# Optimization experiments

Measured on AMD Instinct MI355X. Metric: run time of the kernel, lower is better.

Reference implementation:

```python
import jax, jax.numpy as jnp
import numpy as np

DEPTH = 4
H1 = 64
H2 = 16
NF = 5
L = 10.0
K = 4
DIM = 3
N = 2048
NK = N // 4
FEAT = 1 + 2 * NF * DIM  # r scalar + Nf (cos,sin) pairs of dim components


def _tn(k, shape, std=0.01):
    return jax.random.truncated_normal(k, -2.0, 2.0, shape, jnp.float32) * std


def setup_inputs() -> dict:
    key = jax.random.key(0)
    ks = jax.random.split(key, 16)
    comb0 = 3 * DIM + 3 * FEAT   # combine width at depth 0
    combd = 3 * H1 + 3 * H2      # combine width at later depths
    return {
        "sx": jax.random.uniform(ks[0], (N, DIM), jnp.float32) * L,
        "kpoints": jax.random.normal(ks[1], (2 * NK, DIM), jnp.float32),
        "we0": _tn(ks[2], (comb0, H1)), "be0": jnp.zeros((H1,), jnp.float32),
        "we_rest": _tn(ks[3], (DEPTH - 1, combd, H1)), "be_rest": jnp.zeros((DEPTH - 1, H1), jnp.float32),
        "wee0": _tn(ks[4], (FEAT, H2)), "bee0": jnp.zeros((H2,), jnp.float32),
        "wee_rest": _tn(ks[5], (DEPTH - 2, H2, H2)), "bee_rest": jnp.zeros((DEPTH - 2, H2), jnp.float32),
        "wep0": _tn(ks[6], (FEAT, H2)), "bep0": jnp.zeros((H2,), jnp.float32),
        "wep_rest": _tn(ks[7], (DEPTH - 2, H2, H2)), "bep_rest": jnp.zeros((DEPTH - 2, H2), jnp.float32),
        "orb_w_re": _tn(ks[8], (H1, H1)), "orb_w_im": _tn(ks[9], (H1, H1)),
        "orb_b_re": jnp.zeros((H1,), jnp.float32), "orb_b_im": jnp.zeros((H1,), jnp.float32),
        "w_det": _tn(ks[10], (K, H1, H1)),
        "bf_w": _tn(ks[11], (H1, DIM)),
        "mlp_w1": _tn(ks[12], (DIM, H1)), "mlp_b1": jnp.zeros((H1,), jnp.float32),
        "mlp_w2": _tn(ks[13], (H1, K * (NK - 1))), "mlp_b2": jnp.zeros((K * (NK - 1),), jnp.float32),
    }


def _fourier(rij, r):
    # interleaved [r, cos1, sin1, ..., cosNf, sinNf] like the original
    feats = [r[..., None]]
    for k in range(1, NF + 1):
        ang = (2.0 * np.pi * k / L) * rij
        feats.append(jnp.cos(ang))
        feats.append(jnp.sin(ang))
    return jnp.concatenate(feats, axis=-1)


def _combine(e, ee, ep):
    mm = e.shape[0]
    h = mm // 2
    g1a = jnp.broadcast_to(jnp.mean(e[:h], 0, keepdims=True), e.shape)
    g1b = jnp.broadcast_to(jnp.mean(e[h:], 0, keepdims=True), e.shape)
    g2a = jnp.mean(ee[:h], axis=0)
    g2b = jnp.mean(ee[h:], axis=0)
    g3 = jnp.mean(ep, axis=1)
    return jnp.concatenate([e, g1a, g1b, g2a, g2b, g3], axis=1)


def _forward(sx, kpoints, we0, be0, we_rest, be_rest, wee0, bee0, wee_rest, bee_rest,
             wep0, bep0, wep_rest, bep_rest, orb_w_re, orb_w_im, orb_b_re, orb_b_im,
             w_det, bf_w, mlp_w1, mlp_b1, mlp_w2, mlp_b2):
    n, dim = sx.shape
    m, m2 = n // 2, n // 4
    s, x = sx[:m], sx[m:]
    e = jnp.broadcast_to(kpoints[0][None, :], (m, dim))
    # electron-electron pairwise features (m,m,FEAT)
    rij = x[:, None, :] - x[None, :, :]
    eye = jnp.eye(m, dtype=x.dtype)
    r = jnp.linalg.norm(jnp.sin(np.pi * rij / L) + eye[..., None], axis=-1) * (1.0 - eye) * (L / np.pi)
    ee = _fourier(rij, r)
    # electron-proton pairwise features (m,m,FEAT)
    rij = x[:, None, :] - s[None, :, :]
    r = jnp.linalg.norm(jnp.sin(np.pi * rij / L), axis=-1) * (L / np.pi)
    ep = _fourier(rij, r)
    for d in range(DEPTH - 1):
        f = _combine(e, ee, ep)
        We, be = (we0, be0) if d == 0 else (we_rest[d - 1], be_rest[d - 1])
        Wee, bee = (wee0, bee0) if d == 0 else (wee_rest[d - 1], bee_rest[d - 1])
        Wep, bep = (wep0, bep0) if d == 0 else (wep_rest[d - 1], bep_rest[d - 1])
        e_u = jnp.tanh(f @ We + be)
        ee_u = jnp.tanh(ee @ Wee + bee)
        ep_u = jnp.tanh(ep @ Wep + bep)
        e, ee, ep = (e_u + e, ee_u + ee, ep_u + ep) if d > 0 else (e_u, ee_u, ep_u)
    f = _combine(e, ee, ep)
    e = jnp.tanh(f @ we_rest[-1] + be_rest[-1]) + e
    # complex orbitals and geminal pairing matrix phi: (K, m2, m2)
    orb = e.astype(jnp.complex64) @ (orb_w_re + 1j * orb_w_im) + (orb_b_re + 1j * orb_b_im)
    phi = jnp.einsum('ia,kab,jb->kij', orb[:m2], w_det.astype(jnp.complex64), orb[m2:]) + 1.0
    # backflow coordinates and plane-wave determinant factors
    z = e @ bf_w + x
    nk = kpoints.shape[0] // 2
    norm = 1.0 / L ** (dim / 2)
    D_up = norm * jnp.exp(1j * jnp.einsum('kd,id->ki', kpoints[:nk], z[:m2]))  # (nk, m2)
    D_dn = norm * jnp.exp(1j * jnp.einsum('kd,id->ki', kpoints[nk:], z[m2:]))  # (nk, m2)
    h = jnp.tanh(kpoints[0] @ mlp_w1 + mlp_b1)
    fdet = jax.nn.softplus(h @ mlp_w2 + mlp_b2).reshape(K, nk - 1)
    fdet = jnp.concatenate([jnp.ones((K, 1), fdet.dtype), fdet], axis=1)  # (K, nk)
    D = jnp.einsum('ai,ka,aj->kij', D_up, fdet.astype(D_up.dtype), jnp.conj(D_dn))
    # logdet_matmul: stable log of signed sum of K determinants
    phase, logabs = jnp.linalg.slogdet(D * phi)
    maxl = jnp.max(logabs)
    det = jnp.sum(phase * jnp.exp(logabs - maxl))
    return jnp.log(jnp.abs(det)) + maxl + jnp.log(det / jnp.abs(det))


def reference(sx, kpoints, we0, be0, we_rest, be_rest, wee0, bee0, wee_rest, bee_rest,
              wep0, bep0, wep_rest, bep_rest, orb_w_re, orb_w_im, orb_b_re, orb_b_im,
              w_det, bf_w, mlp_w1, mlp_b1, mlp_w2, mlp_b2):
    return _forward(sx, kpoints, we0, be0, we_rest, be_rest, wee0, bee0, wee_rest, bee_rest,
                    wep0, bep0, wep_rest, bep_rest, orb_w_re, orb_w_im, orb_b_re, orb_b_im,
                    w_det, bf_w, mlp_w1, mlp_b1, mlp_w2, mlp_b2)
```

## Files before the change

kernel.cpp:

```cpp
#include <hip/hip_runtime.h>

typedef unsigned int uint;
typedef unsigned short ushort;

#define M1 1024
#define MH 512
#define PI_F 3.14159265358979323846f
#define LBOX 10.0f
#define NB 32

__device__ __forceinline__ float bf2f(ushort h){ return __uint_as_float(((uint)h)<<16); }
__device__ __forceinline__ ushort f2bf(float f){ uint u = __float_as_uint(f); uint r = (u + 0x7fffu + ((u>>16)&1u))>>16; return (ushort)r; }
__device__ __forceinline__ float ftanh(float x){ float e = __expf(2.f*x); return 1.f - 2.f/(e+1.f); }
__device__ __forceinline__ float2 cmul(float2 a, float2 b){ return make_float2(a.x*b.x - a.y*b.y, a.x*b.y + a.y*b.x); }
__device__ __forceinline__ void cfma(float2& c, float2 a, float2 b){
  c.x = fmaf(a.x,b.x,fmaf(-a.y,b.y,c.x));
  c.y = fmaf(a.x,b.y,fmaf(a.y,b.x,c.y));
}

__device__ __forceinline__ void fourier31(float d0, float d1, float d2, bool diag, float f[31]){
  const float k1 = PI_F / LBOX;
  float s[3], c[3];
  __sincosf(k1*d0, &s[0], &c[0]);
  __sincosf(k1*d1, &s[1], &c[1]);
  __sincosf(k1*d2, &s[2], &c[2]);
  float r = diag ? 0.f : (LBOX/PI_F)*sqrtf(s[0]*s[0]+s[1]*s[1]+s[2]*s[2]);
  f[0] = r;
  float cb[3], sb[3], cc[3], sc[3];
  #pragma unroll
  for (int d=0; d<3; ++d){ cb[d] = 1.f - 2.f*s[d]*s[d]; sb[d] = 2.f*s[d]*c[d]; cc[d]=cb[d]; sc[d]=sb[d]; }
  #pragma unroll
  for (int k=0;k<5;++k){
    #pragma unroll
    for (int d=0; d<3; ++d){ f[1+6*k+d] = cc[d]; f[4+6*k+d] = sc[d]; }
    if (k<4){
      #pragma unroll
      for (int d=0; d<3; ++d){
        float nc = cc[d]*cb[d]-sc[d]*sb[d];
        float ns = sc[d]*cb[d]+cc[d]*sb[d];
        cc[d]=nc; sc[d]=ns;
      }
    }
  }
}

__global__ void k_zero(float* __restrict__ p, int n){
  int i = blockIdx.x*256 + threadIdx.x;
  int st = gridDim.x*256;
  for (; i<n; i+=st) p[i] = 0.f;
}

__global__ void k_iota(int* __restrict__ rowmap){
  int q = blockIdx.x*256 + threadIdx.x;
  rowmap[q] = q & 511;
}

__global__ __launch_bounds__(256) void k_pair0(const float* __restrict__ sx, const float* __restrict__ W,
                                               const float* __restrict__ b, ushort* __restrict__ out, int is_ee,
                                               float* __restrict__ gA, float* __restrict__ gB){
  int bx = blockIdx.x;
  int i = bx >> 2;
  int chunk = bx & 3;
  int j = (chunk << 8) + threadIdx.x;
  const float* xs = sx + 3*M1;
  float xi0 = xs[3*i], xi1 = xs[3*i+1], xi2 = xs[3*i+2];
  const float* oth = is_ee ? xs : sx;
  float y0 = oth[3*j], y1 = oth[3*j+1], y2 = oth[3*j+2];
  float f[31];
  fourier31(xi0-y0, xi1-y1, xi2-y2, is_ee && (i==j), f);
  float acc[16];
  #pragma unroll
  for (int o=0;o<16;++o) acc[o] = b[o];
  #pragma unroll
  for (int c=0;c<31;++c){ float fv = f[c];
    #pragma unroll
    for (int o=0;o<16;++o) acc[o] = fmaf(fv, W[c*16+o], acc[o]);
  }
  uint u[8];
  #pragma unroll
  for (int h=0;h<8;++h){
    ushort lo = f2bf(ftanh(acc[2*h]));
    ushort hi = f2bf(ftanh(acc[2*h+1]));
    u[h] = (uint)lo | ((uint)hi<<16);
  }
  uint4* dst = (uint4*)(out + ((size_t)i*M1 + j)*16);
  dst[0] = make_uint4(u[0],u[1],u[2],u[3]);
  dst[1] = make_uint4(u[4],u[5],u[6],u[7]);
  __shared__ float buf[256*33];
  #pragma unroll
  for (int c=0;c<31;++c) buf[threadIdx.x*33+c] = f[c];
  __syncthreads();
  #pragma unroll
  for (int s=128; s>0; s>>=1){
    if (threadIdx.x < s){
      #pragma unroll
      for (int c=0;c<31;++c) buf[threadIdx.x*33+c] += buf[(threadIdx.x+s)*33+c];
    }
    __syncthreads();
  }
  if (threadIdx.x < 31){
    float* g = (is_ee && chunk >= 2) ? gB : gA;
    atomicAdd(&g[i*31+threadIdx.x], buf[threadIdx.x]);
  }
}

__global__ __launch_bounds__(256) void k_pairU(ushort* __restrict__ ten, const float* __restrict__ W,
                                               const float* __restrict__ b){
  size_t base = ((size_t)blockIdx.x*256 + threadIdx.x)*16;
  uint4 a0 = ((uint4*)(ten+base))[0];
  uint4 a1 = ((uint4*)(ten+base))[1];
  uint uu[8] = {a0.x,a0.y,a0.z,a0.w,a1.x,a1.y,a1.z,a1.w};
  float v[16];
  #pragma unroll
  for (int h=0;h<8;++h){ v[2*h] = bf2f((ushort)(uu[h]&0xffffu)); v[2*h+1] = bf2f((ushort)(uu[h]>>16)); }
  float acc[16];
  #pragma unroll
  for (int o=0;o<16;++o) acc[o] = b[o];
  #pragma unroll
  for (int c=0;c<16;++c){ float fv = v[c];
    #pragma unroll
    for (int o=0;o<16;++o) acc[o] = fmaf(fv, W[c*16+o], acc[o]);
  }
  uint w[8];
  #pragma unroll
  for (int h=0;h<8;++h){
    float q0 = ftanh(acc[2*h]) + v[2*h];
    float q1 = ftanh(acc[2*h+1]) + v[2*h+1];
    w[h] = (uint)f2bf(q0) | ((uint)f2bf(q1)<<16);
  }
  ((uint4*)(ten+base))[0] = make_uint4(w[0],w[1],w[2],w[3]);
  ((uint4*)(ten+base))[1] = make_uint4(w[4],w[5],w[6],w[7]);
}

__global__ __launch_bounds__(256) void k_gee(const ushort* __restrict__ ten, float* __restrict__ gA, float* __restrict__ gB){
  int jb = blockIdx.x >> 3;
  int ic = blockIdx.x & 7;
  int jl = threadIdx.x & 63;
  int iq = threadIdx.x >> 6;
  int j = jb*64 + jl;
  float acc[16];
  #pragma unroll
  for (int c=0;c<16;++c) acc[c]=0.f;
  for (int s=0;s<32;++s){
    int i = ic*128 + iq + 4*s;
    const uint4* src = (const uint4*)(ten + ((size_t)i*M1 + j)*16);
    uint4 a0 = src[0], a1 = src[1];
    uint uu[8]={a0.x,a0.y,a0.z,a0.w,a1.x,a1.y,a1.z,a1.w};
    #pragma unroll
    for (int h=0;h<8;++h){ acc[2*h]+=bf2f((ushort)(uu[h]&0xffffu)); acc[2*h+1]+=bf2f((ushort)(uu[h]>>16)); }
  }
  __shared__ float red[4][64][16];
  #pragma unroll
  for (int c=0;c<16;++c) red[iq][jl][c]=acc[c];
  __syncthreads();
  if (iq==0){
    float* out = (ic<4)? gA : gB;
    #pragma unroll
    for (int c=0;c<16;++c){
      float t = red[0][jl][c]+red[1][jl][c]+red[2][jl][c]+red[3][jl][c];
      atomicAdd(&out[j*16+c], t);
    }
  }
}

__global__ __launch_bounds__(256) void k_gep(const ushort* __restrict__ ten, float* __restrict__ g3){
  int ib = blockIdx.x;
  int il = threadIdx.x >> 6;
  int jl = threadIdx.x & 63;
  int i = ib*4 + il;
  float acc[16];
  #pragma unroll
  for (int c=0;c<16;++c) acc[c]=0.f;
  for (int s=0;s<16;++s){
    int j = jl + 64*s;
    const uint4* src = (const uint4*)(ten + ((size_t)i*M1 + j)*16);
    uint4 a0 = src[0], a1 = src[1];
    uint uu[8]={a0.x,a0.y,a0.z,a0.w,a1.x,a1.y,a1.z,a1.w};
    #pragma unroll
    for (int h=0;h<8;++h){ acc[2*h]+=bf2f((ushort)(uu[h]&0xffffu)); acc[2*h+1]+=bf2f((ushort)(uu[h]>>16)); }
  }
  __shared__ float red[4][64][16];
  #pragma unroll
  for (int c=0;c<16;++c) red[il][jl][c]=acc[c];
  __syncthreads();
  if (jl < 16){
    int c = jl;
    float t=0.f;
    for (int q=0;q<64;++q) t += red[il][q][c];
    g3[i*16+c] = t;
  }
}

__global__ __launch_bounds__(256) void k_e0(const float* __restrict__ kp, const float* __restrict__ g2a,
    const float* __restrict__ g2b, const float* __restrict__ g3, const float* __restrict__ W,
    const float* __restrict__ b, float* __restrict__ eout, float* __restrict__ g1out){
  int p = blockIdx.x*4 + (threadIdx.x>>6);
  int o = threadIdx.x & 63;
  float acc = b[o];
  #pragma unroll
  for (int d=0; d<3; ++d){
    acc = fmaf(kp[d], W[d*64+o] + W[(d+3)*64+o] + W[(d+6)*64+o], acc);
  }
  const float i512 = 1.f/512.f, i1024 = 1.f/1024.f;
  #pragma unroll
  for (int c=0;c<31;++c){
    float sg = (c!=0 && ((c-1)%6)>=3) ? -i512 : i512;
    acc = fmaf(g2a[p*31+c]*sg, W[(9+c)*64+o], acc);
  }
  #pragma unroll
  for (int c=0;c<31;++c){
    float sg = (c!=0 && ((c-1)%6)>=3) ? -i512 : i512;
    acc = fmaf(g2b[p*31+c]*sg, W[(40+c)*64+o], acc);
  }
  #pragma unroll
  for (int c=0;c<31;++c) acc = fmaf(g3[p*31+c]*i1024, W[(71+c)*64+o], acc);
  float v = ftanh(acc);
  eout[p*64+o] = v;
  atomicAdd(&g1out[(p<MH?0:64)+o], v);
}

__global__ __launch_bounds__(256) void k_eupd(const float* __restrict__ eprev, float* __restrict__ eout,
    const float* __restrict__ W, const float* __restrict__ b, const float* __restrict__ g1in,
    const float* __restrict__ g2a, const float* __restrict__ g2b, const float* __restrict__ g3,
    float* __restrict__ g1out){
  int p = blockIdx.x*4 + (threadIdx.x>>6);
  int o = threadIdx.x & 63;
  const float i512 = 1.f/512.f, i1024 = 1.f/1024.f;
  float acc = b[o];
  #pragma unroll 8
  for (int c=0;c<64;++c) acc = fmaf(eprev[p*64+c], W[c*64+o], acc);
  #pragma unroll 8
  for (int c=0;c<64;++c) acc = fmaf(g1in[c]*i512, W[(64+c)*64+o], acc);
  #pragma unroll 8
  for (int c=0;c<64;++c) acc = fmaf(g1in[64+c]*i512, W[(128+c)*64+o], acc);
  #pragma unroll
  for (int c=0;c<16;++c) acc = fmaf(g2a[p*16+c]*i512, W[(192+c)*64+o], acc);
  #pragma unroll
  for (int c=0;c<16;++c) acc = fmaf(g2b[p*16+c]*i512, W[(208+c)*64+o], acc);
  #pragma unroll
  for (int c=0;c<16;++c) acc = fmaf(g3[p*16+c]*i1024, W[(224+c)*64+o], acc);
  float v = ftanh(acc) + eprev[p*64+o];
  eout[p*64+o] = v;
  if (g1out) atomicAdd(&g1out[(p<MH?0:64)+o], v);
}

__global__ __launch_bounds__(256) void k_orbz(const float* __restrict__ e4, const float* __restrict__ Wre,
    const float* __restrict__ Wim, const float* __restrict__ bre, const float* __restrict__ bim,
    const float* __restrict__ bfw, const float* __restrict__ sx, float* __restrict__ ore,
    float* __restrict__ oim, float* __restrict__ z){
  int p = blockIdx.x*4 + (threadIdx.x>>6);
  int o = threadIdx.x & 63;
  float ar = bre[o], ai = bim[o];
  #pragma unroll 8
  for (int a=0;a<64;++a){ float ev = e4[p*64+a]; ar = fmaf(ev, Wre[a*64+o], ar); ai = fmaf(ev, Wim[a*64+o], ai); }
  ore[p*64+o]=ar; oim[p*64+o]=ai;
  if (o<3){
    float zz = sx[(M1+p)*3+o];
    for (int a=0;a<64;++a) zz = fmaf(e4[p*64+a], bfw[a*3+o], zz);
    z[p*3+o]=zz;
  }
}

__global__ __launch_bounds__(256) void k_fdet(const float* __restrict__ kp, const float* __restrict__ w1,
    const float* __restrict__ b1, const float* __restrict__ w2, const float* __restrict__ b2,
    float* __restrict__ fdet){
  __shared__ float hs[64];
  int tid = threadIdx.x;
  if (tid < 64){
    float acc = b1[tid];
    for (int d=0;d<3;++d) acc = fmaf(kp[d], w1[d*64+tid], acc);
    hs[tid] = ftanh(acc);
  }
  __syncthreads();
  int c = blockIdx.x*256 + tid;
  if (c < 2044){
    float acc = b2[c];
    #pragma unroll 8
    for (int o=0;o<64;++o) acc = fmaf(hs[o], w2[o*2044+c], acc);
    float sp = (acc > 20.f) ? acc : log1pf(__expf(acc));
    int kk = c / 511, idx = c % 511;
    fdet[kk*512 + 1 + idx] = sp;
  }
  if (blockIdx.x == 0 && tid < 4) fdet[tid*512] = 1.f;
}

__global__ __launch_bounds__(256) void k_uv(const float* __restrict__ kp, const float* __restrict__ z,
                                            float2* __restrict__ U, float2* __restrict__ V){
  int gid = blockIdx.x*256 + threadIdx.x;
  int sel = gid >> 18;
  int rem = gid & 262143;
  int a = rem >> 9;
  int col = rem & 511;
  const float nrm = 0.031622776601683794f;
  const float* kr = kp + (sel ? (512+a)*3 : a*3);
  const float* zr = z + (sel ? (512+col)*3 : col*3);
  float th = kr[0]*zr[0] + kr[1]*zr[1] + kr[2]*zr[2];
  float s, c; __sincosf(th, &s, &c);
  float2 v = make_float2(nrm*c, nrm*s);
  if (sel) V[a*512+col] = v; else U[a*512+col] = v;
}

__global__ __launch_bounds__(256) void k_T(const float* __restrict__ ore, const float* __restrict__ oim,
                                           const float* __restrict__ wdet, float2* __restrict__ T){
  int k = blockIdx.x >> 7;
  int iblk = blockIdx.x & 127;
  int i = iblk*4 + (threadIdx.x>>6);
  int bc = threadIdx.x & 63;
  __shared__ float wd[4096];
  for (int t = threadIdx.x; t < 4096; t += 256) wd[t] = wdet[k*4096 + t];
  __syncthreads();
  float ar=0.f, ai=0.f;
  #pragma unroll 8
  for (int a=0;a<64;++a){
    float w = wd[a*64+bc];
    ar = fmaf(ore[i*64+a], w, ar);
    ai = fmaf(oim[i*64+a], w, ai);
  }
  T[((size_t)k*512 + i)*64 + bc] = make_float2(ar, ai);
}

__global__ __launch_bounds__(256) void k_M(const float2* __restrict__ U, const float2* __restrict__ V,
    const float* __restrict__ fdet, const float2* __restrict__ T, const float* __restrict__ ore,
    const float* __restrict__ oim, float2* __restrict__ Mb){
  __shared__ float2 sm[4160];
  int k = blockIdx.x >> 8;
  int ty = (blockIdx.x >> 4) & 15;
  int tx = blockIdx.x & 15;
  int ib = ty*32, jb = tx*32;
  int i0 = (threadIdx.x >> 4)*2;
  int j0 = (threadIdx.x & 15)*2;
  const float* fk = fdet + k*512;
  float2 a00={0,0},a01={0,0},a10={0,0},a11={0,0};
  float2* As = sm;
  float2* Bs = sm + 512;
  for (int a0=0; a0<512; a0+=16){
    for (int t = threadIdx.x; t < 512; t += 256){
      int aa = t >> 5, il = t & 31;
      int a = a0 + aa;
      float fv = fk[a];
      float2 u = U[a*512 + ib + il];
      As[t] = make_float2(u.x*fv, u.y*fv);
      float2 v = V[a*512 + jb + il];
      Bs[t] = make_float2(v.x, -v.y);
    }
    __syncthreads();
    #pragma unroll
    for (int aa=0; aa<16; ++aa){
      float2 A0 = As[aa*32+i0], A1 = As[aa*32+i0+1];
      float2 B0 = Bs[aa*32+j0], B1 = Bs[aa*32+j0+1];
      cfma(a00,A0,B0); cfma(a01,A0,B1); cfma(a10,A1,B0); cfma(a11,A1,B1);
    }
    __syncthreads();
  }
  float2* Ts = sm;
  float2* Od = sm + 2080;
  for (int t = threadIdx.x; t < 2048; t += 256){
    int il = t >> 6, bc = t & 63;
    Ts[il*65+bc] = T[((size_t)k*512 + ib + il)*64 + bc];
    int oidx = (512 + jb + il)*64 + bc;
    Od[il*65+bc] = make_float2(ore[oidx], oim[oidx]);
  }
  __syncthreads();
  float2 p00={1,0},p01={1,0},p10={1,0},p11={1,0};
  #pragma unroll 8
  for (int bb=0; bb<64; ++bb){
    float2 T0 = Ts[i0*65+bb], T1 = Ts[(i0+1)*65+bb];
    float2 O0 = Od[j0*65+bb], O1 = Od[(j0+1)*65+bb];
    cfma(p00,T0,O0); cfma(p01,T0,O1); cfma(p10,T1,O0); cfma(p11,T1,O1);
  }
  size_t base = ((size_t)k*512 + ib + i0)*512 + jb + j0;
  Mb[base]     = cmul(a00, p00);
  Mb[base+1]   = cmul(a01, p01);
  Mb[base+512] = cmul(a10, p10);
  Mb[base+513] = cmul(a11, p11);
}

__global__ __launch_bounds__(512)
void k_panel(float2* __restrict__ Mb, float2* __restrict__ LinvG,
             int* __restrict__ rowmap, int* __restrict__ swapc, int col0){
  int k = blockIdx.x;
  float2* Mk = Mb + (size_t)k*512*512;
  int R = 512 - col0;
  int R64 = R < 64 ? R : 64;
  int rl = threadIdx.x;
  bool active = rl < R;
  int wv = rl >> 6;
  __shared__ float2 mir[64*33];
  __shared__ float2 Us[NB*33];
  __shared__ float2 dinv[NB];
  __shared__ float2 Ls[NB*NB];
  __shared__ float2 Yv[NB*NB];
  __shared__ int winslot[NB];
  __shared__ int newposS[64];
  int rm_orig = active ? rowmap[k*512 + col0 + rl] : 0;
  float2 X[NB];
  if (rl >= 64 && active){
    const float4* rp = (const float4*)(Mk + (size_t)rm_orig*512 + col0);
    #pragma unroll
    for (int q=0;q<NB/2;++q){ float4 v = rp[q]; X[2*q]=make_float2(v.x,v.y); X[2*q+1]=make_float2(v.z,v.w); }
  }
  if (wv == 0){
    if (rl < R64){
      const float4* rp = (const float4*)(Mk + (size_t)rm_orig*512 + col0);
      #pragma unroll
      for (int q=0;q<NB/2;++q){
        float4 v = rp[q];
        mir[rl*33+2*q]   = make_float2(v.x,v.y);
        mir[rl*33+2*q+1] = make_float2(v.z,v.w);
      }
    }
    bool done = false;
    int winpos = 0;
    for (int cc=0; cc<NB; ++cc){
      bool cand = (rl < R64) && !done;
      float2 cv = make_float2(0.f,0.f);
      if (cand) cv = mir[rl*33+cc];
      float val = cand ? fmaf(cv.x,cv.x,cv.y*cv.y) : -1.f;
      int idx = rl;
      #pragma unroll
      for (int off=32; off>0; off>>=1){
        float ov = __shfl_xor(val, off);
        int   oi = __shfl_xor(idx, off);
        if (ov > val || (ov == val && oi < idx)){ val = ov; idx = oi; }
      }
      int p = idx;
      if (rl == 0) winslot[cc] = p;
      if (rl == p){ done = true; winpos = cc; }
      float2 dg = mir[p*33+cc];
      float dn = 1.f/fmaf(dg.x,dg.x,dg.y*dg.y);
      float2 inv = make_float2(dg.x*dn, -dg.y*dn);
      if (cand && rl != p){
        float2 l = cmul(cv, inv);
        mir[rl*33+cc] = l;
        for (int j=cc+1; j<NB; ++j){
          float2 pr = mir[p*33+j];
          float2 xv = mir[rl*33+j];
          xv.x = fmaf(-l.x, pr.x, fmaf( l.y, pr.y, xv.x));
          xv.y = fmaf(-l.x, pr.y, fmaf(-l.y, pr.x, xv.y));
          mir[rl*33+j] = xv;
        }
      }
    }
    unsigned long long nwmask = __ballot(rl < R64 && !done);
    int np = 0;
    if (rl < R64){
      np = done ? winpos : (NB + (int)__popcll(nwmask & ((1ull<<rl)-1ull)));
      newposS[rl] = np;
      rowmap[k*512 + col0 + np] = rm_orig;
      float4* wp = (float4*)(Mk + (size_t)rm_orig*512 + col0);
      #pragma unroll
      for (int q=0;q<NB/2;++q){
        float2 a = mir[rl*33+2*q], bq = mir[rl*33+2*q+1];
        wp[q] = make_float4(a.x,a.y,bq.x,bq.y);
      }
    }
    {
      int cnt = 0;
      for (int t=0;t<R64;++t){
        int nt = newposS[t];
        if (rl < R64 && t > rl && nt < np) cnt++;
      }
      #pragma unroll
      for (int off=32; off>0; off>>=1) cnt += __shfl_xor(cnt, off);
      if (rl == 0) swapc[k] += cnt;
    }
    if (rl < NB){
      int ws = winslot[rl];
      #pragma unroll
      for (int j=0;j<NB;++j){
        float2 v = mir[ws*33+j];
        Us[rl*33+j] = v;
        float2 lv;
        if      (j <  rl) lv = v;
        else if (j == rl) lv = make_float2(1.f,0.f);
        else              lv = make_float2(0.f,0.f);
        Ls[rl*NB+j] = lv;
      }
      float2 d = Us[rl*33+rl];
      float dn = 1.f/fmaf(d.x,d.x,d.y*d.y);
      dinv[rl] = make_float2(d.x*dn, -d.y*dn);
    }
  }
  __syncthreads();
  if (rl >= 64 && active){
    #pragma unroll
    for (int j=0;j<NB;++j){
      float2 t = X[j];
      #pragma unroll
      for (int q=0;q<NB;++q){
        if (q < j){
          float2 u = Us[q*33+j];
          t.x = fmaf(-X[q].x, u.x, fmaf( X[q].y, u.y, t.x));
          t.y = fmaf(-X[q].x, u.y, fmaf(-X[q].y, u.x, t.y));
        }
      }
      X[j] = cmul(t, dinv[j]);
    }
    float4* wp = (float4*)(Mk + (size_t)rm_orig*512 + col0);
    #pragma unroll
    for (int q=0;q<NB/2;++q) wp[q] = make_float4(X[2*q].x,X[2*q].y,X[2*q+1].x,X[2*q+1].y);
  }
  if (rl < NB){
    for (int i=0;i<NB;++i){
      float2 acc = (i==rl)? make_float2(1.f,0.f) : make_float2(0.f,0.f);
      for (int q=rl; q<i; ++q){
        float2 lv = Ls[i*NB+q];
        float2 yv = Yv[q*NB+rl];
        acc.x = fmaf(-lv.x, yv.x, fmaf( lv.y, yv.y, acc.x));
        acc.y = fmaf(-lv.x, yv.y, fmaf(-lv.y, yv.x, acc.y));
      }
      Yv[i*NB+rl] = acc;
    }
  }
  __syncthreads();
  {
    float4* dst = (float4*)(LinvG + (size_t)k*(NB*NB));
    const float4* src = (const float4*)Yv;
    for (int q=rl; q<NB*NB/2; q+=blockDim.x) dst[q] = src[q];
  }
}

__global__ __launch_bounds__(256) void k_gemm(float2* __restrict__ Mb, const float2* __restrict__ LinvG,
                                              const int* __restrict__ rowmap, int col0){
  int k = blockIdx.z;
  float2* Mk = Mb + (size_t)k*512*512;
  int e0 = col0 + NB;
  int r0 = e0 + blockIdx.x*32;
  int j0c = e0 + blockIdx.y*32;
  int tid = threadIdx.x;
  int jl = tid & 31, rg = tid >> 5;
  __shared__ float2 As[NB*33];
  __shared__ float2 Bs[NB*33];
  __shared__ float2 Av[NB*33];
  __shared__ float2 Li[NB*NB];
  __shared__ int prA[32];
  __shared__ int prB[NB];
  if (tid < 32) prA[tid] = rowmap[k*512 + r0 + tid];
  else if (tid < 64) prB[tid-32] = rowmap[k*512 + col0 + (tid-32)];
  {
    const float4* src = (const float4*)(LinvG + (size_t)k*(NB*NB));
    float4* dst = (float4*)Li;
    for (int q=tid; q<NB*NB/2; q+=256) dst[q] = src[q];
  }
  __syncthreads();
  #pragma unroll
  for (int s=0;s<4;++s){
    int a = rg + 8*s;
    Av[a*33 + jl] = Mk[(size_t)prB[a]*512 + j0c + jl];
  }
  for (int t=tid; t<1024; t+=256){
    int rl = t >> 5, kk = t & 31;
    As[kk*33+rl] = Mk[(size_t)prA[rl]*512 + col0 + kk];
  }
  __syncthreads();
  #pragma unroll
  for (int s=0;s<4;++s){
    int m = rg + 8*s;
    float2 acc = make_float2(0.f,0.f);
    #pragma unroll 8
    for (int a=0;a<NB;++a) cfma(acc, Li[m*NB+a], Av[a*33+jl]);
    Bs[m*33+jl] = acc;
  }
  __syncthreads();
  int i0 = (tid >> 4)*2, j0 = (tid & 15)*2;
  float2 a00={0,0},a01={0,0},a10={0,0},a11={0,0};
  #pragma unroll 16
  for (int kk=0;kk<NB;++kk){
    float2 A0 = As[kk*33+i0], A1 = As[kk*33+i0+1];
    float2 B0 = Bs[kk*33+j0], B1 = Bs[kk*33+j0+1];
    cfma(a00,A0,B0); cfma(a01,A0,B1); cfma(a10,A1,B0); cfma(a11,A1,B1);
  }
  size_t ro0 = (size_t)prA[i0]*512 + j0c + j0;
  size_t ro1 = (size_t)prA[i0+1]*512 + j0c + j0;
  float2 c0 = Mk[ro0];   c0.x-=a00.x; c0.y-=a00.y; Mk[ro0]=c0;
  float2 c1 = Mk[ro0+1]; c1.x-=a01.x; c1.y-=a01.y; Mk[ro0+1]=c1;
  float2 c2 = Mk[ro1];   c2.x-=a10.x; c2.y-=a10.y; Mk[ro1]=c2;
  float2 c3 = Mk[ro1+1]; c3.x-=a11.x; c3.y-=a11.y; Mk[ro1+1]=c3;
}

__global__ void k_det(const float2* __restrict__ Mb, const int* __restrict__ rowmap,
                      const int* __restrict__ swapc, float* __restrict__ out, int out_size){
  int tid = threadIdx.x;
  int k = tid >> 6, lane = tid & 63;
  const float2* Mk = Mb + (size_t)k*512*512;
  double la = 0.0, ang = 0.0;
  for (int q=0;q<8;++q){
    int i = lane*8 + q;
    int pr = rowmap[k*512 + i];
    float2 u = Mk[(size_t)pr*512+i];
    double re = (double)u.x, im = (double)u.y;
    la += 0.5*log(re*re + im*im);
    ang += atan2(im, re);
  }
  #pragma unroll
  for (int off=32; off>0; off>>=1){
    la += __shfl_down(la, off);
    ang += __shfl_down(ang, off);
  }
  __shared__ double las[4], angs[4];
  if (lane==0){
    las[k] = la;
    angs[k] = ang + 3.14159265358979323846*(double)(swapc[k] & 1);
  }
  __syncthreads();
  if (tid==0){
    double mx = las[0];
    for (int q=1;q<4;++q) mx = fmax(mx, las[q]);
    double sre=0.0, sim=0.0;
    for (int q=0;q<4;++q){
      double w = exp(las[q]-mx);
      sre += w*cos(angs[q]);
      sim += w*sin(angs[q]);
    }
    double mag = sqrt(sre*sre+sim*sim);
    out[0] = (float)(log(mag)+mx);
    if (out_size > 1) out[1] = (float)atan2(sim, sre);
    for (int q=2;q<out_size;++q) out[q] = 0.f;
  }
}

extern "C" void kernel_launch(void* const* d_in, const int* in_sizes, int n_in,
                              void* d_out, int out_size, void* d_ws, size_t ws_size,
                              hipStream_t stream){
  const float* sx   = (const float*)d_in[0];
  const float* kp   = (const float*)d_in[1];
  const float* we0  = (const float*)d_in[2];
  const float* be0  = (const float*)d_in[3];
  const float* weR  = (const float*)d_in[4];
  const float* beR  = (const float*)d_in[5];
  const float* wee0 = (const float*)d_in[6];
  const float* bee0 = (const float*)d_in[7];
  const float* weeR = (const float*)d_in[8];
  const float* beeR = (const float*)d_in[9];
  const float* wep0 = (const float*)d_in[10];
  const float* bep0 = (const float*)d_in[11];
  const float* wepR = (const float*)d_in[12];
  const float* bepR = (const float*)d_in[13];
  const float* owre = (const float*)d_in[14];
  const float* owim = (const float*)d_in[15];
  const float* obre = (const float*)d_in[16];
  const float* obim = (const float*)d_in[17];
  const float* wdet = (const float*)d_in[18];
  const float* bfw  = (const float*)d_in[19];
  const float* mw1  = (const float*)d_in[20];
  const float* mb1  = (const float*)d_in[21];
  const float* mw2  = (const float*)d_in[22];
  const float* mb2  = (const float*)d_in[23];

  char* ws = (char*)d_ws;
  size_t off = 0;
  auto alloc = [&](size_t bytes)->char*{
    char* p = ws + off;
    off = (off + bytes + 255) & ~(size_t)255;
    return p;
  };
  ushort* ee   = (ushort*)alloc(33554432);
  ushort* ep   = (ushort*)alloc(33554432);
  float2* Mb   = (float2*)alloc(8388608);
  float2* U    = (float2*)alloc(2097152);
  float2* V    = (float2*)alloc(2097152);
  float2* T    = (float2*)alloc(1048576);
  float*  eS   = (float*)alloc(1048576);
  float*  ore  = (float*)alloc(262144);
  float*  oim  = (float*)alloc(262144);
  float*  z    = (float*)alloc(12288);
  float*  fdet = (float*)alloc(8192);
  float2* Linv = (float2*)alloc(131072);
  int*    rowmap = (int*)alloc(8192);
  char*   zst  = ws + off;
  float*  g2a0 = (float*)alloc(126976);
  float*  g2b0 = (float*)alloc(126976);
  float*  g30  = (float*)alloc(126976);
  float*  geeA = (float*)alloc(196608);
  float*  geeB = (float*)alloc(196608);
  float*  gep  = (float*)alloc(196608);
  float*  g1s  = (float*)alloc(1536);
  int*    swpc = (int*)alloc(16);
  int zn = (int)(((char*)(swpc+4) - zst)/4);

  float* e1 = eS;           float* e2 = eS + 65536;
  float* e3 = eS + 131072;  float* e4 = eS + 196608;
  float* geeA1 = geeA;      float* geeA2 = geeA+16384; float* geeA3 = geeA+32768;
  float* geeB1 = geeB;      float* geeB2 = geeB+16384; float* geeB3 = geeB+32768;
  float* gep1  = gep;       float* gep2  = gep+16384;  float* gep3  = gep+32768;
  float* g1s1 = g1s; float* g1s2 = g1s+128; float* g1s3 = g1s+256;

  k_zero<<<256,256,0,stream>>>((float*)zst, zn);
  k_iota<<<8,256,0,stream>>>(rowmap);
  k_pair0<<<4096,256,0,stream>>>(sx, wee0, bee0, ee, 1, g2a0, g2b0);
  k_pair0<<<4096,256,0,stream>>>(sx, wep0, bep0, ep, 0, g30, g30);
  k_e0<<<256,256,0,stream>>>(kp, g2a0, g2b0, g30, we0, be0, e1, g1s1);
  k_gee<<<128,256,0,stream>>>(ee, geeA1, geeB1);
  k_gep<<<256,256,0,stream>>>(ep, gep1);
  k_eupd<<<256,256,0,stream>>>(e1, e2, weR, beR, g1s1, geeA1, geeB1, gep1, g1s2);
  k_pairU<<<4096,256,0,stream>>>(ee, weeR, beeR);
  k_pairU<<<4096,256,0,stream>>>(ep, wepR, bepR);
  k_gee<<<128,256,0,stream>>>(ee, geeA2, geeB2);
  k_gep<<<256,256,0,stream>>>(ep, gep2);
  k_eupd<<<256,256,0,stream>>>(e2, e3, weR+240*64, beR+64, g1s2, geeA2, geeB2, gep2, g1s3);
  k_pairU<<<4096,256,0,stream>>>(ee, weeR+256, beeR+16);
  k_pairU<<<4096,256,0,stream>>>(ep, wepR+256, bepR+16);
  k_gee<<<128,256,0,stream>>>(ee, geeA3, geeB3);
  k_gep<<<256,256,0,stream>>>(ep, gep3);
  k_eupd<<<256,256,0,stream>>>(e3, e4, weR+2*240*64, beR+128, g1s3, geeA3, geeB3, gep3, nullptr);
  k_orbz<<<256,256,0,stream>>>(e4, owre, owim, obre, obim, bfw, sx, ore, oim, z);
  k_fdet<<<8,256,0,stream>>>(kp, mw1, mb1, mw2, mb2, fdet);
  k_uv<<<2048,256,0,stream>>>(kp, z, U, V);
  k_T<<<512,256,0,stream>>>(ore, oim, wdet, T);
  k_M<<<1024,256,0,stream>>>(U, V, fdet, T, ore, oim, Mb);
  for (int tpan=0;tpan<16;++tpan){
    int col0 = tpan*NB;
    int R = 512 - col0;
    int Rpad = (R + 63) & ~63;
    k_panel<<<4, Rpad, 0, stream>>>(Mb, Linv, rowmap, swpc, col0);
    if (tpan < 15){
      int nch = 15 - tpan;
      k_gemm<<<dim3(nch,nch,4),256,0,stream>>>(Mb, Linv, rowmap, col0);
    }
  }
  k_det<<<1,256,0,stream>>>(Mb, rowmap, swpc, (float*)d_out, out_size);
  (void)in_sizes; (void)n_in; (void)ws_size;
}
```

Measured before the change: 1.843 ms.

## Fuse ep row-sum reductions into pair kernels and retile k_M to 64x64

The separate k_gep pass, which re-read the whole ep tensor to sum rows, is removed. Those row sums are now built inside k_pair0 and k_pairU through a block reduction plus atomics. The k_M complex GEMM is retiled from 32x32 to 64x64 tiles with 4x4 register blocking per thread, and the zero and iota init kernels are merged into one. This saves three full tensor reads and some launches, at the cost of extra shared-memory reductions in the pair kernels and atomic summation order that is no longer deterministic.

```diff
diff --git a/kernel.cpp b/kernel.cpp
--- a/kernel.cpp
+++ b/kernel.cpp
@@ -44,20 +44,16 @@
   }
 }
 
-__global__ void k_zero(float* __restrict__ p, int n){
+__global__ void k_init(float* __restrict__ p, int n, int* __restrict__ rowmap){
   int i = blockIdx.x*256 + threadIdx.x;
-  int st = gridDim.x*256;
-  for (; i<n; i+=st) p[i] = 0.f;
-}
-
-__global__ void k_iota(int* __restrict__ rowmap){
-  int q = blockIdx.x*256 + threadIdx.x;
-  rowmap[q] = q & 511;
+  if (i < 2048) rowmap[i] = i & 511;
+  for (int q=i; q<n; q+=gridDim.x*256) p[q] = 0.f;
 }
 
 __global__ __launch_bounds__(256) void k_pair0(const float* __restrict__ sx, const float* __restrict__ W,
                                                const float* __restrict__ b, ushort* __restrict__ out, int is_ee,
-                                               float* __restrict__ gA, float* __restrict__ gB){
+                                               float* __restrict__ gA, float* __restrict__ gB,
+                                               float* __restrict__ gH){
   int bx = blockIdx.x;
   int i = bx >> 2;
   int chunk = bx & 3;
@@ -76,36 +72,41 @@
     #pragma unroll
     for (int o=0;o<16;++o) acc[o] = fmaf(fv, W[c*16+o], acc[o]);
   }
+  float hv[16];
+  #pragma unroll
+  for (int o=0;o<16;++o) hv[o] = ftanh(acc[o]);
   uint u[8];
   #pragma unroll
   for (int h=0;h<8;++h){
-    ushort lo = f2bf(ftanh(acc[2*h]));
-    ushort hi = f2bf(ftanh(acc[2*h+1]));
-    u[h] = (uint)lo | ((uint)hi<<16);
+    u[h] = (uint)f2bf(hv[2*h]) | ((uint)f2bf(hv[2*h+1])<<16);
   }
   uint4* dst = (uint4*)(out + ((size_t)i*M1 + j)*16);
   dst[0] = make_uint4(u[0],u[1],u[2],u[3]);
   dst[1] = make_uint4(u[4],u[5],u[6],u[7]);
-  __shared__ float buf[256*33];
-  #pragma unroll
-  for (int c=0;c<31;++c) buf[threadIdx.x*33+c] = f[c];
+  __shared__ float buf[256*49];
+  #pragma unroll
+  for (int c=0;c<31;++c) buf[threadIdx.x*49+c] = f[c];
+  #pragma unroll
+  for (int c=0;c<16;++c) buf[threadIdx.x*49+31+c] = hv[c];
   __syncthreads();
   #pragma unroll
   for (int s=128; s>0; s>>=1){
     if (threadIdx.x < s){
       #pragma unroll
-      for (int c=0;c<31;++c) buf[threadIdx.x*33+c] += buf[(threadIdx.x+s)*33+c];
+      for (int c=0;c<47;++c) buf[threadIdx.x*49+c] += buf[(threadIdx.x+s)*49+c];
     }
     __syncthreads();
   }
   if (threadIdx.x < 31){
     float* g = (is_ee && chunk >= 2) ? gB : gA;
     atomicAdd(&g[i*31+threadIdx.x], buf[threadIdx.x]);
+  } else if (threadIdx.x < 47 && gH){
+    atomicAdd(&gH[i*16 + (threadIdx.x-31)], buf[threadIdx.x]);
   }
 }
 
 __global__ __launch_bounds__(256) void k_pairU(ushort* __restrict__ ten, const float* __restrict__ W,
-                                               const float* __restrict__ b){
+                                               const float* __restrict__ b, float* __restrict__ gOut){
   size_t base = ((size_t)blockIdx.x*256 + threadIdx.x)*16;
   uint4 a0 = ((uint4*)(ten+base))[0];
   uint4 a1 = ((uint4*)(ten+base))[1];
@@ -121,15 +122,34 @@
     #pragma unroll
     for (int o=0;o<16;++o) acc[o] = fmaf(fv, W[c*16+o], acc[o]);
   }
+  float nv[16];
+  #pragma unroll
+  for (int o=0;o<16;++o) nv[o] = ftanh(acc[o]) + v[o];
   uint w[8];
   #pragma unroll
   for (int h=0;h<8;++h){
-    float q0 = ftanh(acc[2*h]) + v[2*h];
-    float q1 = ftanh(acc[2*h+1]) + v[2*h+1];
-    w[h] = (uint)f2bf(q0) | ((uint)f2bf(q1)<<16);
+    w[h] = (uint)f2bf(nv[2*h]) | ((uint)f2bf(nv[2*h+1])<<16);
   }
   ((uint4*)(ten+base))[0] = make_uint4(w[0],w[1],w[2],w[3]);
   ((uint4*)(ten+base))[1] = make_uint4(w[4],w[5],w[6],w[7]);
+  __shared__ float buf[256*17];
+  if (gOut){
+    #pragma unroll
+    for (int c=0;c<16;++c) buf[threadIdx.x*17+c] = nv[c];
+    __syncthreads();
+    #pragma unroll
+    for (int s=128; s>0; s>>=1){
+      if (threadIdx.x < s){
+        #pragma unroll
+        for (int c=0;c<16;++c) buf[threadIdx.x*17+c] += buf[(threadIdx.x+s)*17+c];
+      }
+      __syncthreads();
+    }
+    if (threadIdx.x < 16){
+      int i = blockIdx.x >> 2;
+      atomicAdd(&gOut[i*16 + threadIdx.x], buf[threadIdx.x]);
+    }
+  }
 }
 
 __global__ __launch_bounds__(256) void k_gee(const ushort* __restrict__ ten, float* __restrict__ gA, float* __restrict__ gB){
@@ -160,34 +180,6 @@
       float t = red[0][jl][c]+red[1][jl][c]+red[2][jl][c]+red[3][jl][c];
       atomicAdd(&out[j*16+c], t);
     }
-  }
-}
-
-__global__ __launch_bounds__(256) void k_gep(const ushort* __restrict__ ten, float* __restrict__ g3){
-  int ib = blockIdx.x;
-  int il = threadIdx.x >> 6;
-  int jl = threadIdx.x & 63;
-  int i = ib*4 + il;
-  float acc[16];
-  #pragma unroll
-  for (int c=0;c<16;++c) acc[c]=0.f;
-  for (int s=0;s<16;++s){
-    int j = jl + 64*s;
-    const uint4* src = (const uint4*)(ten + ((size_t)i*M1 + j)*16);
-    uint4 a0 = src[0], a1 = src[1];
-    uint uu[8]={a0.x,a0.y,a0.z,a0.w,a1.x,a1.y,a1.z,a1.w};
-    #pragma unroll
-    for (int h=0;h<8;++h){ acc[2*h]+=bf2f((ushort)(uu[h]&0xffffu)); acc[2*h+1]+=bf2f((ushort)(uu[h]>>16)); }
-  }
-  __shared__ float red[4][64][16];
-  #pragma unroll
-  for (int c=0;c<16;++c) red[il][jl][c]=acc[c];
-  __syncthreads();
-  if (jl < 16){
-    int c = jl;
-    float t=0.f;
-    for (int q=0;q<64;++q) t += red[il][q][c];
-    g3[i*16+c] = t;
   }
 }
 
@@ -322,57 +314,81 @@
 __global__ __launch_bounds__(256) void k_M(const float2* __restrict__ U, const float2* __restrict__ V,
     const float* __restrict__ fdet, const float2* __restrict__ T, const float* __restrict__ ore,
     const float* __restrict__ oim, float2* __restrict__ Mb){
-  __shared__ float2 sm[4160];
-  int k = blockIdx.x >> 8;
-  int ty = (blockIdx.x >> 4) & 15;
-  int tx = blockIdx.x & 15;
-  int ib = ty*32, jb = tx*32;
-  int i0 = (threadIdx.x >> 4)*2;
-  int j0 = (threadIdx.x & 15)*2;
+  __shared__ float2 As[16*66];
+  __shared__ float2 Bs[16*66];
+  int k = blockIdx.z;
+  int ib = blockIdx.y * 64, jb = blockIdx.x * 64;
+  int tid = threadIdx.x;
+  int ti = (tid >> 4) * 4;
+  int tj = (tid & 15) * 4;
   const float* fk = fdet + k*512;
-  float2 a00={0,0},a01={0,0},a10={0,0},a11={0,0};
-  float2* As = sm;
-  float2* Bs = sm + 512;
+  float2 acc[4][4];
+  #pragma unroll
+  for (int a=0;a<4;++a){
+    #pragma unroll
+    for (int b=0;b<4;++b) acc[a][b] = make_float2(0.f,0.f);
+  }
   for (int a0=0; a0<512; a0+=16){
-    for (int t = threadIdx.x; t < 512; t += 256){
-      int aa = t >> 5, il = t & 31;
+    #pragma unroll
+    for (int s=0;s<4;++s){
+      int t = tid + s*256;
+      int aa = t >> 6, il = t & 63;
       int a = a0 + aa;
       float fv = fk[a];
       float2 u = U[a*512 + ib + il];
-      As[t] = make_float2(u.x*fv, u.y*fv);
+      As[aa*66+il] = make_float2(u.x*fv, u.y*fv);
       float2 v = V[a*512 + jb + il];
-      Bs[t] = make_float2(v.x, -v.y);
+      Bs[aa*66+il] = make_float2(v.x, -v.y);
     }
     __syncthreads();
     #pragma unroll
-    for (int aa=0; aa<16; ++aa){
-      float2 A0 = As[aa*32+i0], A1 = As[aa*32+i0+1];
-      float2 B0 = Bs[aa*32+j0], B1 = Bs[aa*32+j0+1];
-      cfma(a00,A0,B0); cfma(a01,A0,B1); cfma(a10,A1,B0); cfma(a11,A1,B1);
+    for (int aa=0;aa<16;++aa){
+      float2 Av[4], Bv[4];
+      #pragma unroll
+      for (int q=0;q<4;++q){ Av[q] = As[aa*66+ti+q]; Bv[q] = Bs[aa*66+tj+q]; }
+      #pragma unroll
+      for (int qi=0;qi<4;++qi){
+        #pragma unroll
+        for (int qj=0;qj<4;++qj) cfma(acc[qi][qj], Av[qi], Bv[qj]);
+      }
     }
     __syncthreads();
   }
-  float2* Ts = sm;
-  float2* Od = sm + 2080;
-  for (int t = threadIdx.x; t < 2048; t += 256){
-    int il = t >> 6, bc = t & 63;
-    Ts[il*65+bc] = T[((size_t)k*512 + ib + il)*64 + bc];
-    int oidx = (512 + jb + il)*64 + bc;
-    Od[il*65+bc] = make_float2(ore[oidx], oim[oidx]);
-  }
-  __syncthreads();
-  float2 p00={1,0},p01={1,0},p10={1,0},p11={1,0};
-  #pragma unroll 8
-  for (int bb=0; bb<64; ++bb){
-    float2 T0 = Ts[i0*65+bb], T1 = Ts[(i0+1)*65+bb];
-    float2 O0 = Od[j0*65+bb], O1 = Od[(j0+1)*65+bb];
-    cfma(p00,T0,O0); cfma(p01,T0,O1); cfma(p10,T1,O0); cfma(p11,T1,O1);
-  }
-  size_t base = ((size_t)k*512 + ib + i0)*512 + jb + j0;
-  Mb[base]     = cmul(a00, p00);
-  Mb[base+1]   = cmul(a01, p01);
-  Mb[base+512] = cmul(a10, p10);
-  Mb[base+513] = cmul(a11, p11);
+  float2 ph[4][4];
+  #pragma unroll
+  for (int a=0;a<4;++a){
+    #pragma unroll
+    for (int b=0;b<4;++b) ph[a][b] = make_float2(1.f,0.f);
+  }
+  for (int b0=0; b0<64; b0+=16){
+    #pragma unroll
+    for (int s=0;s<4;++s){
+      int t = tid + s*256;
+      int aa = t >> 6, il = t & 63;
+      As[aa*66+il] = T[((size_t)k*512 + ib + il)*64 + b0 + aa];
+      int oidx = (512 + jb + il)*64 + b0 + aa;
+      Bs[aa*66+il] = make_float2(ore[oidx], oim[oidx]);
+    }
+    __syncthreads();
+    #pragma unroll
+    for (int aa=0;aa<16;++aa){
+      float2 Av[4], Bv[4];
+      #pragma unroll
+      for (int q=0;q<4;++q){ Av[q] = As[aa*66+ti+q]; Bv[q] = Bs[aa*66+tj+q]; }
+      #pragma unroll
+      for (int qi=0;qi<4;++qi){
+        #pragma unroll
+        for (int qj=0;qj<4;++qj) cfma(ph[qi][qj], Av[qi], Bv[qj]);
+      }
+    }
+    __syncthreads();
+  }
+  #pragma unroll
+  for (int qi=0;qi<4;++qi){
+    size_t ro = ((size_t)k*512 + ib + ti + qi)*512 + jb + tj;
+    #pragma unroll
+    for (int qj=0;qj<4;++qj) Mb[ro+qj] = cmul(acc[qi][qj], ph[qi][qj]);
+  }
 }
 
 __global__ __launch_bounds__(512)
@@ -685,29 +701,25 @@
   float* gep1  = gep;       float* gep2  = gep+16384;  float* gep3  = gep+32768;
   float* g1s1 = g1s; float* g1s2 = g1s+128; float* g1s3 = g1s+256;
 
-  k_zero<<<256,256,0,stream>>>((float*)zst, zn);
-  k_iota<<<8,256,0,stream>>>(rowmap);
-  k_pair0<<<4096,256,0,stream>>>(sx, wee0, bee0, ee, 1, g2a0, g2b0);
-  k_pair0<<<4096,256,0,stream>>>(sx, wep0, bep0, ep, 0, g30, g30);
+  k_init<<<256,256,0,stream>>>((float*)zst, zn, rowmap);
+  k_pair0<<<4096,256,0,stream>>>(sx, wee0, bee0, ee, 1, g2a0, g2b0, nullptr);
+  k_pair0<<<4096,256,0,stream>>>(sx, wep0, bep0, ep, 0, g30, g30, gep1);
   k_e0<<<256,256,0,stream>>>(kp, g2a0, g2b0, g30, we0, be0, e1, g1s1);
   k_gee<<<128,256,0,stream>>>(ee, geeA1, geeB1);
-  k_gep<<<256,256,0,stream>>>(ep, gep1);
   k_eupd<<<256,256,0,stream>>>(e1, e2, weR, beR, g1s1, geeA1, geeB1, gep1, g1s2);
-  k_pairU<<<4096,256,0,stream>>>(ee, weeR, beeR);
-  k_pairU<<<4096,256,0,stream>>>(ep, wepR, bepR);
+  k_pairU<<<4096,256,0,stream>>>(ee, weeR, beeR, nullptr);
+  k_pairU<<<4096,256,0,stream>>>(ep, wepR, bepR, gep2);
   k_gee<<<128,256,0,stream>>>(ee, geeA2, geeB2);
-  k_gep<<<256,256,0,stream>>>(ep, gep2);
   k_eupd<<<256,256,0,stream>>>(e2, e3, weR+240*64, beR+64, g1s2, geeA2, geeB2, gep2, g1s3);
-  k_pairU<<<4096,256,0,stream>>>(ee, weeR+256, beeR+16);
-  k_pairU<<<4096,256,0,stream>>>(ep, wepR+256, bepR+16);
+  k_pairU<<<4096,256,0,stream>>>(ee, weeR+256, beeR+16, nullptr);
+  k_pairU<<<4096,256,0,stream>>>(ep, wepR+256, bepR+16, gep3);
   k_gee<<<128,256,0,stream>>>(ee, geeA3, geeB3);
-  k_gep<<<256,256,0,stream>>>(ep, gep3);
   k_eupd<<<256,256,0,stream>>>(e3, e4, weR+2*240*64, beR+128, g1s3, geeA3, geeB3, gep3, nullptr);
   k_orbz<<<256,256,0,stream>>>(e4, owre, owim, obre, obim, bfw, sx, ore, oim, z);
   k_fdet<<<8,256,0,stream>>>(kp, mw1, mb1, mw2, mb2, fdet);
   k_uv<<<2048,256,0,stream>>>(kp, z, U, V);
   k_T<<<512,256,0,stream>>>(ore, oim, wdet, T);
-  k_M<<<1024,256,0,stream>>>(U, V, fdet, T, ore, oim, Mb);
+  k_M<<<dim3(8,8,4),256,0,stream>>>(U, V, fdet, T, ore, oim, Mb);
   for (int tpan=0;tpan<16;++tpan){
     int col0 = tpan*NB;
     int R = 512 - col0;
```

Result: slower. 1.894 ms (+2.8%).
